# Performance work log

Measured on AMD Instinct MI355X. Metric: run time of the kernel, lower is better.

Reference implementation:

```python
import jax, jax.numpy as jnp
import numpy as np

SR = 8                      # search_range
MO = 2 * SR + 1             # max_offset = 17
NC = MO * MO                # 289 cost-volume channels


def _l2_normalize(x, eps=1e-12):
    # torch F.normalize(p=2, dim=1): x / max(||x||_2, eps)
    n = jnp.sqrt(jnp.sum(x * x, axis=1, keepdims=True))
    return x / jnp.maximum(n, eps)


def _conv2d(x, w, b, pad, groups=1):
    out = jax.lax.conv_general_dilated(
        x, w, window_strides=(1, 1), padding=[(pad, pad), (pad, pad)],
        feature_group_count=groups,
        dimension_numbers=('NCHW', 'OIHW', 'NCHW'))
    return out + b[None, :, None, None]


def _cost_volume(x1, x2, sr, norm_both=False):
    x1 = _l2_normalize(x1)
    if norm_both:
        x2 = _l2_normalize(x2)
    bs, c, h, w = x1.shape
    padded = jnp.pad(x2, ((0, 0), (0, 0), (sr, sr), (sr, sr)))
    mo = 2 * sr + 1
    # offsets in (j outer, i inner) order, matching the original double loop
    jj, ii = jnp.meshgrid(jnp.arange(mo), jnp.arange(mo), indexing='ij')
    offs = jnp.stack([jj.reshape(-1), ii.reshape(-1)], axis=-1)  # [mo^2, 2]

    def step(carry, off):
        sl = jax.lax.dynamic_slice(padded, (0, 0, off[0], off[1]), (bs, c, h, w))
        return carry, jnp.mean(x1 * sl, axis=1)  # [bs, h, w]

    _, cv = jax.lax.scan(step, None, offs)       # [mo^2, bs, h, w]
    cv = jnp.transpose(cv, (1, 0, 2, 3))          # [bs, mo^2, h, w]
    return jax.nn.leaky_relu(cv, 0.1)


def setup_inputs() -> dict:
    key = jax.random.key(0)
    ks = jax.random.split(key, 8)
    bs, c, h, w = 4, 256, 64, 64
    scale = 0.05
    return {
        'f1': jax.random.normal(ks[0], (bs, c, h, w), jnp.float32),
        'f2': jax.random.normal(ks[1], (bs, c, h, w), jnp.float32),
        'att_w': jax.random.normal(ks[2], (NC, 1, 7, 7), jnp.float32) * scale,
        'att_b': jax.random.normal(ks[3], (NC,), jnp.float32) * scale,
        'agg1_w': jax.random.normal(ks[4], (NC // 2, NC, 3, 3), jnp.float32) * scale,
        'agg1_b': jax.random.normal(ks[5], (NC // 2,), jnp.float32) * scale,
        'agg2_w': jax.random.normal(ks[6], (49, NC // 2, 3, 3), jnp.float32) * scale,
        'agg2_b': jax.random.normal(ks[7], (49,), jnp.float32) * scale,
    }


def reference(f1, f2, att_w, att_b, agg1_w, agg1_b, agg2_w, agg2_b):
    match_vol = _cost_volume(f1, f2, SR, norm_both=False)          # [bs,289,h,w]
    att = _conv2d(match_vol, att_w, att_b, pad=3, groups=NC)       # depthwise 7x7
    att_vol = match_vol * att
    h1 = jax.nn.relu(_conv2d(att_vol, agg1_w, agg1_b, pad=1))      # Conv(289->144,3)
    out = jax.nn.relu(_conv2d(h1, agg2_w, agg2_b, pad=1))          # Conv(144->49,3)
    return out
```

## Files before the change

### kernel.cpp

```cpp
#include <hip/hip_runtime.h>
#include <hip/hip_bf16.h>

#define BS   4
#define C    256
#define HW   4096
#define NPIX 16384
#define NCH  289
#define MO   17
#define PH   80
#define PW   80
#define C1   144
#define C2   49
#define ASTR 264
#define ICP  320
#define IC2  160
#define A2STR 168
#define CVP  70
#define CVC  320
#define CH64 72

typedef __bf16  bf16x8 __attribute__((ext_vector_type(8)));
typedef float   f32x4  __attribute__((ext_vector_type(4)));
typedef unsigned short us8 __attribute__((ext_vector_type(8)));

__global__ void fused_norm_transpose(const float* __restrict__ f1,
                                     unsigned short* __restrict__ dst) {
    __shared__ float tileT[32 * 257];
    __shared__ float invS[32];
    int blk = blockIdx.x;
    int pblk = blk & 127, b = blk >> 7;
    int p0 = pblk * 32;
    int t = threadIdx.x;
    int tx = t & 31, ty = t >> 5;
    const float* s = f1 + (size_t)b * C * HW;
#pragma unroll
    for (int i = 0; i < 32; ++i) {
        int c = ty + 8 * i;
        tileT[tx * 257 + c] = s[(size_t)c * HW + p0 + tx];
    }
    __syncthreads();
    int lane = t & 63, wave = t >> 6;
    int px = wave * 8 + (lane >> 3);
    int l = lane & 7;
    float ssum = 0.f;
#pragma unroll
    for (int j = 0; j < 32; ++j) {
        float v = tileT[px * 257 + l + 8 * j];
        ssum += v * v;
    }
    ssum += __shfl_xor(ssum, 1);
    ssum += __shfl_xor(ssum, 2);
    ssum += __shfl_xor(ssum, 4);
    if (l == 0) invS[px] = 1.0f / fmaxf(sqrtf(ssum), 1e-12f);
    __syncthreads();
#pragma unroll 4
    for (int p = 0; p < 32; ++p) {
        float v = tileT[p * 257 + t] * invS[p];
        __hip_bfloat16 hb = __float2bfloat16(v);
        dst[((size_t)b * HW + p0 + p) * C + t] = *(unsigned short*)&hb;
    }
}

__global__ void transpose_pad_kernel(const float* __restrict__ src,
                                     unsigned short* __restrict__ dst) {
    __shared__ float tile[32][33];
    int blk = blockIdx.x;
    int pblk = blk & 127;
    int cblk = (blk >> 7) & 7;
    int b    = blk >> 10;
    int tx = threadIdx.x & 31, ty = threadIdx.x >> 5;
    int c0 = cblk * 32, p0 = pblk * 32;
    const float* s = src + (size_t)b * C * HW;
#pragma unroll
    for (int i = 0; i < 4; ++i) {
        int c = c0 + ty + 8 * i;
        tile[ty + 8 * i][tx] = s[(size_t)c * HW + p0 + tx];
    }
    __syncthreads();
#pragma unroll
    for (int i = 0; i < 4; ++i) {
        int p = p0 + ty + 8 * i;
        float v = tile[tx][ty + 8 * i];
        int c = c0 + tx;
        int h = p >> 6, w = p & 63;
        __hip_bfloat16 hb = __float2bfloat16(v);
        dst[(((size_t)b * PH + h + 8) * PW + (w + 8)) * C + c] = *(unsigned short*)&hb;
    }
}

__global__ void halo_zero(unsigned short* __restrict__ p, int H, int halo, int Cc) {
    int W = H;
    int inter = H - 2 * halo;
    int total_pos = H * W - inter * inter;
    int chunks = Cc >> 3;
    size_t tot = (size_t)total_pos * chunks * BS;
    size_t idx = (size_t)blockIdx.x * 256 + threadIdx.x;
    if (idx >= tot) return;
    int c8 = (int)(idx % chunks);
    size_t r = idx / chunks;
    int pos = (int)(r % total_pos);
    int b = (int)(r / total_pos);
    int h, w;
    int topbot = 2 * halo * W;
    if (pos < halo * W) { h = pos / W; w = pos % W; }
    else if (pos < topbot) { int q = pos - halo * W; h = H - halo + q / W; w = q % W; }
    else {
        int q = pos - topbot;
        int row = q / (2 * halo), off = q % (2 * halo);
        h = halo + row;
        w = (off < halo) ? off : (W - 2 * halo + off);
    }
    us8 z = {0, 0, 0, 0, 0, 0, 0, 0};
    *(us8*)&p[(((size_t)b * H + h) * W + w) * Cc + c8 * 8] = z;
}

__global__ void rearrange_w1_bf(const float* __restrict__ w, unsigned short* __restrict__ wb) {
    int idx = blockIdx.x * 256 + threadIdx.x;
    if (idx >= 9 * C1 * ICP) return;
    int tap = idx / (C1 * ICP);
    int r = idx - tap * (C1 * ICP);
    int oc = r / ICP;
    int ic = r - oc * ICP;
    float v = (ic < NCH) ? w[((size_t)(oc * NCH + ic)) * 9 + tap] : 0.f;
    __hip_bfloat16 hb = __float2bfloat16(v);
    wb[idx] = *(unsigned short*)&hb;
}
__global__ void rearrange_w2_bf(const float* __restrict__ w, unsigned short* __restrict__ wb) {
    int idx = blockIdx.x * 256 + threadIdx.x;
    if (idx >= 9 * 64 * IC2) return;
    int tap = idx / (64 * IC2);
    int r = idx - tap * (64 * IC2);
    int oc = r / IC2;
    int ic = r - oc * IC2;
    float v = (oc < C2 && ic < C1) ? w[((size_t)(oc * C1 + ic)) * 9 + tap] : 0.f;
    __hip_bfloat16 hb = __float2bfloat16(v);
    wb[idx] = *(unsigned short*)&hb;
}
__global__ void rearrange_dw_pad(const float* __restrict__ w, float* __restrict__ wr) {
    int idx = blockIdx.x * 256 + threadIdx.x;
    if (idx >= 49 * CVC) return;
    int tap = idx / CVC;
    int ch = idx - tap * CVC;
    wr[idx] = (ch < NCH) ? w[ch * 49 + tap] : 0.f;
}

__global__ void cv_mfma_kernel(const unsigned short* __restrict__ x1b,
                               const unsigned short* __restrict__ x2b,
                               unsigned short* __restrict__ cvp) {
    __shared__ __align__(16) unsigned short x2s[2][32 * ASTR];
    int i = blockIdx.x;
    int xcd = i & 7;
    int j = i >> 3;
    int hq = xcd * 2 + (j & 1);
    int jj = j >> 1;
    int wseg = jj & 3;
    int b = jj >> 2;
    int h0 = hq * 4;
    int w0 = wseg * 16;
    int t = threadIdx.x;
    int wave = t >> 6, lane = t & 63;
    int lrow = lane & 15, quad = lane >> 4;
    int h = h0 + wave;

    const unsigned short* x1p = x1b + ((size_t)b * HW + h * 64 + w0) * C;
    bf16x8 a[8];
#pragma unroll
    for (int kk = 0; kk < 8; ++kk)
        a[kk] = *(const bf16x8*)&x1p[(size_t)lrow * C + kk * 32 + quad * 8];

    const unsigned short* x2base = x2b + (size_t)b * PH * PW * C;

    {
        const unsigned short* rowp = x2base + ((size_t)h0 * PW + w0) * C;
#pragma unroll
        for (int s = 0; s < 4; ++s) {
            int v = t + s * 256;
            int col = v >> 5, ch8 = v & 31;
            *(us8*)&x2s[0][col * ASTR + ch8 * 8] = *(const us8*)&rowp[(size_t)col * C + ch8 * 8];
        }
    }
    __syncthreads();

    for (int rr = 0; rr < 20; ++rr) {
        us8 pr[4];
        bool dop = (rr + 1 < 20);
        if (dop) {
            const unsigned short* rowp = x2base + ((size_t)(h0 + rr + 1) * PW + w0) * C;
#pragma unroll
            for (int s = 0; s < 4; ++s) {
                int v = t + s * 256;
                int col = v >> 5, ch8 = v & 31;
                pr[s] = *(const us8*)&rowp[(size_t)col * C + ch8 * 8];
            }
        }

        int dj = rr - wave;
        if ((unsigned)dj <= 16u) {
            const unsigned short* xs = x2s[rr & 1];
#pragma unroll
            for (int c = 0; c < 2; ++c) {
                f32x4 acc = {0.f, 0.f, 0.f, 0.f};
#pragma unroll
                for (int kk = 0; kk < 8; ++kk) {
                    bf16x8 bb = *(const bf16x8*)&xs[(c * 16 + lrow) * ASTR + kk * 32 + quad * 8];
                    acc = __builtin_amdgcn_mfma_f32_16x16x32_bf16(a[kk], bb, acc, 0, 0, 0);
                }
#pragma unroll
                for (int r = 0; r < 4; ++r) {
                    int px_l = quad * 4 + r;
                    int di = c * 16 + lrow - px_l;
                    if ((unsigned)di <= 16u) {
                        float v = acc[r] * (1.0f / 256.0f);
                        v = (v > 0.f) ? v : 0.1f * v;
                        __hip_bfloat16 hb = __float2bfloat16(v);
                        cvp[(((size_t)b * CVP + h + 3) * CVP + (w0 + px_l + 3)) * CVC + dj * MO + di] =
                            *(unsigned short*)&hb;
                    }
                }
            }
        }

        if (dop) {
            unsigned short* dst = x2s[(rr + 1) & 1];
#pragma unroll
            for (int s = 0; s < 4; ++s) {
                int v = t + s * 256;
                int col = v >> 5, ch8 = v & 31;
                *(us8*)&dst[col * ASTR + ch8 * 8] = pr[s];
            }
            __syncthreads();
        }
    }
}

__global__ void dw_att_tiled(const unsigned short* __restrict__ cvp,
                             const float* __restrict__ wdwp,
                             const float* __restrict__ att_b, unsigned short* __restrict__ av_pad) {
    __shared__ float actS[14 * 14 * 64];
    __shared__ float wdwS[49 * 64];
    int i = blockIdx.x;
    int ty = i & 7;
    int j = i >> 3;
    int cc = j % 5;
    int rest = j / 5;
    int tx = rest & 7, b = rest >> 3;
    int x0 = tx * 8, y0 = ty * 8;
    int c0 = cc * 64;
    int t = threadIdx.x;

    const unsigned short* cvb = cvp + (((size_t)b * CVP + y0) * CVP + x0) * CVC + c0;
    for (int v = t; v < 14 * 14 * 8; v += 256) {
        int rc = v >> 3, c8v = v & 7;
        int yy = rc / 14, xx = rc - yy * 14;
        bf16x8 raw = *(const bf16x8*)&cvb[((size_t)yy * CVP + xx) * CVC + c8v * 8];
        f32x4 lo, hi;
#pragma unroll
        for (int e = 0; e < 4; ++e) { lo[e] = (float)raw[e]; hi[e] = (float)raw[e + 4]; }
        *(f32x4*)&actS[rc * 64 + c8v * 8] = lo;
        *(f32x4*)&actS[rc * 64 + c8v * 8 + 4] = hi;
    }
    for (int v = t; v < 49 * 64; v += 256) {
        int tap = v >> 6, ch = v & 63;
        wdwS[v] = wdwp[tap * CVC + c0 + ch];
    }
    __syncthreads();

    int ch_l = t & 63, pgrp = t >> 6;
    int ch = c0 + ch_l;
    float bv = (ch < NCH) ? att_b[ch] : 0.f;
    float acc[16];
#pragma unroll
    for (int ii = 0; ii < 16; ++ii) acc[ii] = bv;

    for (int dy = 0; dy < 7; ++dy) {
#pragma unroll
        for (int dx = 0; dx < 7; ++dx) {
            float wv = wdwS[(dy * 7 + dx) * 64 + ch_l];
#pragma unroll
            for (int ii = 0; ii < 16; ++ii) {
                int py = pgrp * 2 + (ii >> 3), px = ii & 7;
                float a = actS[((py + dy) * 14 + (px + dx)) * 64 + ch_l];
                acc[ii] += a * wv;
            }
        }
    }

    if (ch < NCH) {
#pragma unroll
        for (int ii = 0; ii < 16; ++ii) {
            int py = pgrp * 2 + (ii >> 3), px = ii & 7;
            float c0v = actS[((py + 3) * 14 + (px + 3)) * 64 + ch_l];
            __hip_bfloat16 hb = __float2bfloat16(c0v * acc[ii]);
            av_pad[(((size_t)b * 66 + y0 + py + 1) * 66 + (x0 + px + 1)) * ICP + ch] =
                *(unsigned short*)&hb;
        }
    }
}

__global__ void agg1_mfma_kernel(const unsigned short* __restrict__ av_pad,
                                 const unsigned short* __restrict__ wb1,
                                 const float* __restrict__ bias,
                                 unsigned short* __restrict__ h1p) {
    __shared__ __align__(16) unsigned short aS2[2][66 * CH64];
    __shared__ __align__(16) unsigned short bS[2][C1 * CH64];
    int i = blockIdx.x;
    int xcd = i & 7;
    int j = i >> 3;
    int h = xcd * 8 + (j & 7);
    int b = j >> 3;
    int t = threadIdx.x;
    int wave = t >> 6, lane = t & 63;
    int lrow = lane & 15, quad = lane >> 4;
    int ot0 = (wave == 0) ? 0 : (wave * 2 + 1);
    int nt  = (wave == 0) ? 3 : 2;

    f32x4 acc[4][3];
#pragma unroll
    for (int m = 0; m < 4; ++m)
#pragma unroll
        for (int ii = 0; ii < 3; ++ii) acc[m][ii] = (f32x4){0.f, 0.f, 0.f, 0.f};

    const unsigned short* avb = av_pad + (((size_t)b * 66 + h) * 66) * ICP;

    {
        const unsigned short* arow = avb;
#pragma unroll
        for (int s = 0; s < 2; ++s) {
            int v = t + s * 256;
            *(us8*)&aS2[0][(v >> 3) * CH64 + (v & 7) * 8] =
                *(const us8*)&arow[(size_t)(v >> 3) * ICP + (v & 7) * 8];
        }
        if (t < 16) {
            int v = t + 512;
            *(us8*)&aS2[0][(v >> 3) * CH64 + (v & 7) * 8] =
                *(const us8*)&arow[(size_t)(v >> 3) * ICP + (v & 7) * 8];
        }
#pragma unroll
        for (int s = 0; s < 4; ++s) {
            int v = t + s * 256;
            *(us8*)&bS[0][(v >> 3) * CH64 + (v & 7) * 8] =
                *(const us8*)&wb1[(size_t)(v >> 3) * ICP + (v & 7) * 8];
        }
        if (t < 128) {
            int v = t + 1024;
            *(us8*)&bS[0][(v >> 3) * CH64 + (v & 7) * 8] =
                *(const us8*)&wb1[(size_t)(v >> 3) * ICP + (v & 7) * 8];
        }
    }
    __syncthreads();

    for (int k = 0; k < 45; ++k) {
        int rr = k % 15;
        int dx = rr % 3;
        int abuf = (k / 3) & 1, bbuf = k & 1;

        us8 br[5], ar[3];
        int kn = k + 1;
        bool do_b = (kn < 45);
        bool do_a = do_b && (kn % 3 == 0);
        int dyn = kn / 15, rn = kn % 15;
        int ccin = rn / 3, dxn = rn % 3;
        if (do_b) {
            const unsigned short* wt = wb1 + ((size_t)(dyn * 3 + dxn) * C1) * ICP + ccin * 64;
#pragma unroll
            for (int s = 0; s < 4; ++s) {
                int v = t + s * 256;
                br[s] = *(const us8*)&wt[(size_t)(v >> 3) * ICP + (v & 7) * 8];
            }
            if (t < 128) {
                int v = t + 1024;
                br[4] = *(const us8*)&wt[(size_t)(v >> 3) * ICP + (v & 7) * 8];
            }
        }
        if (do_a) {
            const unsigned short* arow = avb + (size_t)dyn * 66 * ICP + ccin * 64;
#pragma unroll
            for (int s = 0; s < 2; ++s) {
                int v = t + s * 256;
                ar[s] = *(const us8*)&arow[(size_t)(v >> 3) * ICP + (v & 7) * 8];
            }
            if (t < 16) {
                int v = t + 512;
                ar[2] = *(const us8*)&arow[(size_t)(v >> 3) * ICP + (v & 7) * 8];
            }
        }

        const unsigned short* aP = aS2[abuf];
        const unsigned short* bP = bS[bbuf];
#pragma unroll
        for (int cc2 = 0; cc2 < 2; ++cc2) {
            bf16x8 bfr[3];
#pragma unroll
            for (int ii = 0; ii < 3; ++ii)
                if (ii < nt)
                    bfr[ii] = *(const bf16x8*)&bP[((ot0 + ii) * 16 + lrow) * CH64 + cc2 * 32 + quad * 8];
#pragma unroll
            for (int m = 0; m < 4; ++m) {
                bf16x8 af = *(const bf16x8*)&aP[(m * 16 + lrow + dx) * CH64 + cc2 * 32 + quad * 8];
#pragma unroll
                for (int ii = 0; ii < 3; ++ii)
                    if (ii < nt)
                        acc[m][ii] = __builtin_amdgcn_mfma_f32_16x16x32_bf16(af, bfr[ii], acc[m][ii], 0, 0, 0);
            }
        }

        if (do_b) {
            unsigned short* dst = bS[bbuf ^ 1];
#pragma unroll
            for (int s = 0; s < 4; ++s) {
                int v = t + s * 256;
                *(us8*)&dst[(v >> 3) * CH64 + (v & 7) * 8] = br[s];
            }
            if (t < 128) {
                int v = t + 1024;
                *(us8*)&dst[(v >> 3) * CH64 + (v & 7) * 8] = br[4];
            }
        }
        if (do_a) {
            unsigned short* dst = aS2[abuf ^ 1];
#pragma unroll
            for (int s = 0; s < 2; ++s) {
                int v = t + s * 256;
                *(us8*)&dst[(v >> 3) * CH64 + (v & 7) * 8] = ar[s];
            }
            if (t < 16) {
                int v = t + 512;
                *(us8*)&dst[(v >> 3) * CH64 + (v & 7) * 8] = ar[2];
            }
        }
        if (do_b) __syncthreads();
    }

    size_t rowbase = ((size_t)b * 66 + h + 1) * 66;
#pragma unroll
    for (int m = 0; m < 4; ++m)
#pragma unroll
        for (int ii = 0; ii < 3; ++ii)
            if (ii < nt) {
                int oc = (ot0 + ii) * 16 + lrow;
                float bv = bias[oc];
#pragma unroll
                for (int r = 0; r < 4; ++r) {
                    int w = m * 16 + quad * 4 + r;
                    float val = fmaxf(acc[m][ii][r] + bv, 0.f);
                    __hip_bfloat16 hb = __float2bfloat16(val);
                    h1p[(rowbase + (w + 1)) * IC2 + oc] = *(unsigned short*)&hb;
                }
            }
}

__global__ void agg2_mfma_kernel(const unsigned short* __restrict__ h1p,
                                 const unsigned short* __restrict__ wb2,
                                 const float* __restrict__ bias, float* __restrict__ out) {
    __shared__ __align__(16) unsigned short aS[66 * A2STR];
    __shared__ __align__(16) unsigned short bS[64 * A2STR];
    int i = blockIdx.x;
    int xcd = i & 7;
    int j = i >> 3;
    int h = xcd * 8 + (j & 7);
    int b = j >> 3;
    int t = threadIdx.x;
    int wave = t >> 6, lane = t & 63;
    int lrow = lane & 15, quad = lane >> 4;
    int pt = wave;

    f32x4 acc[4];
#pragma unroll
    for (int ot = 0; ot < 4; ++ot) acc[ot] = (f32x4){0.f, 0.f, 0.f, 0.f};

    const unsigned short* h1b = h1p + (((size_t)b * 66 + h) * 66) * IC2;

    for (int dy = 0; dy < 3; ++dy) {
        __syncthreads();
        const unsigned short* arow = h1b + (size_t)dy * 66 * IC2;
        for (int v = t; v < 66 * (IC2 / 8); v += 256) {
            int col = v / (IC2 / 8);
            int c8 = v - col * (IC2 / 8);
            *(us8*)&aS[col * A2STR + c8 * 8] = *(const us8*)&arow[col * IC2 + c8 * 8];
        }
        for (int dx = 0; dx < 3; ++dx) {
            int tap = dy * 3 + dx;
            if (dx != 0) __syncthreads();
            const unsigned short* wtap = wb2 + (size_t)tap * 64 * IC2;
            for (int v = t; v < 64 * (IC2 / 8); v += 256) {
                int oc = v / (IC2 / 8);
                int c8 = v - oc * (IC2 / 8);
                *(us8*)&bS[oc * A2STR + c8 * 8] = *(const us8*)&wtap[(size_t)oc * IC2 + c8 * 8];
            }
            __syncthreads();
#pragma unroll
            for (int cc = 0; cc < 5; ++cc) {
                bf16x8 af = *(const bf16x8*)&aS[(pt * 16 + lrow + dx) * A2STR + cc * 32 + quad * 8];
#pragma unroll
                for (int ot = 0; ot < 4; ++ot) {
                    bf16x8 bfr = *(const bf16x8*)&bS[(ot * 16 + lrow) * A2STR + cc * 32 + quad * 8];
                    acc[ot] = __builtin_amdgcn_mfma_f32_16x16x32_bf16(af, bfr, acc[ot], 0, 0, 0);
                }
            }
        }
    }

#pragma unroll
    for (int ot = 0; ot < 4; ++ot) {
        int o = ot * 16 + lrow;
        if (o < C2) {
            float bv = bias[o];
#pragma unroll
            for (int r = 0; r < 4; ++r) {
                int w = pt * 16 + quad * 4 + r;
                out[((size_t)b * C2 + o) * HW + h * 64 + w] = fmaxf(acc[ot][r] + bv, 0.f);
            }
        }
    }
}

extern "C" void kernel_launch(void* const* d_in, const int* in_sizes, int n_in,
                              void* d_out, int out_size, void* d_ws, size_t ws_size,
                              hipStream_t stream) {
    const float* f1    = (const float*)d_in[0];
    const float* f2    = (const float*)d_in[1];
    const float* att_w = (const float*)d_in[2];
    const float* att_b = (const float*)d_in[3];
    const float* w1    = (const float*)d_in[4];
    const float* b1    = (const float*)d_in[5];
    const float* w2    = (const float*)d_in[6];
    const float* b2    = (const float*)d_in[7];
    float* out = (float*)d_out;

    char* wsb = (char*)d_ws;
    size_t off = 0;
    float* wdwp = (float*)(wsb + off); off += (size_t)49 * CVC * 4;
    off = (off + 15) & ~(size_t)15;
    unsigned short* x1bf = (unsigned short*)(wsb + off); off += (size_t)NPIX * C * 2;
    unsigned short* x2bf = (unsigned short*)(wsb + off); off += (size_t)BS * PH * PW * C * 2;
    unsigned short* cvp  = (unsigned short*)(wsb + off); off += (size_t)BS * CVP * CVP * CVC * 2;
    unsigned short* avp  = (unsigned short*)(wsb + off); off += (size_t)BS * 66 * 66 * ICP * 2;
    unsigned short* wb1  = (unsigned short*)(wsb + off); off += (size_t)9 * C1 * ICP * 2;
    unsigned short* h1p  = (unsigned short*)(wsb + off); off += (size_t)BS * 66 * 66 * IC2 * 2;
    unsigned short* wb2  = (unsigned short*)(wsb + off); off += (size_t)9 * 64 * IC2 * 2;
    if (ws_size < off) return;

    halo_zero<<<1152, 256, 0, stream>>>(x2bf, PH, 8, C);
    halo_zero<<<503, 256, 0, stream>>>(cvp, CVP, 3, CVC);
    halo_zero<<<163, 256, 0, stream>>>(avp, 66, 1, ICP);
    halo_zero<<<82, 256, 0, stream>>>(h1p, 66, 1, IC2);

    fused_norm_transpose<<<512, 256, 0, stream>>>(f1, x1bf);
    transpose_pad_kernel<<<4096, 256, 0, stream>>>(f2, x2bf);

    rearrange_w1_bf<<<(9 * C1 * ICP + 255) / 256, 256, 0, stream>>>(w1, wb1);
    rearrange_w2_bf<<<(9 * 64 * IC2 + 255) / 256, 256, 0, stream>>>(w2, wb2);
    rearrange_dw_pad<<<(49 * CVC + 255) / 256, 256, 0, stream>>>(att_w, wdwp);

    cv_mfma_kernel<<<256, 256, 0, stream>>>(x1bf, x2bf, cvp);
    dw_att_tiled<<<1280, 256, 0, stream>>>(cvp, wdwp, att_b, avp);
    agg1_mfma_kernel<<<256, 256, 0, stream>>>(avp, wb1, b1, h1p);
    agg2_mfma_kernel<<<256, 256, 0, stream>>>(h1p, wb2, b2, out);
}
```

Before: 213.3 us.

## Merge prep kernels into one launch and double-buffer agg2 loads

Seven small setup launches (halo zeroing and weight rearrangement) become one block-indexed prep kernel, which removes launch overhead. The agg2 conv now walks 27 steps of 64-channel chunks with double-buffered LDS. The next step's activation and weight chunks are prefetched into registers during the current MFMA work, and there is one barrier per step. The h1 channel stride is padded to 192 so the chunks divide evenly, which adds a few zero-channel MFMAs and raises register pressure.

New measurement: 195.5 us. 8.4% less time.

```diff
diff --git a/kernel.cpp b/kernel.cpp
--- a/kernel.cpp
+++ b/kernel.cpp
@@ -13,8 +13,7 @@
 #define C2   49
 #define ASTR 264
 #define ICP  320
-#define IC2  160
-#define A2STR 168
+#define IC3  192
 #define CVP  70
 #define CVC  320
 #define CH64 72
@@ -88,13 +87,14 @@
     }
 }
 
-__global__ void halo_zero(unsigned short* __restrict__ p, int H, int halo, int Cc) {
+__device__ __forceinline__ void halo_zero_dev(unsigned short* p, int H, int halo,
+                                              int Cc, int blk, int t) {
     int W = H;
     int inter = H - 2 * halo;
     int total_pos = H * W - inter * inter;
     int chunks = Cc >> 3;
     size_t tot = (size_t)total_pos * chunks * BS;
-    size_t idx = (size_t)blockIdx.x * 256 + threadIdx.x;
+    size_t idx = (size_t)blk * 256 + t;
     if (idx >= tot) return;
     int c8 = (int)(idx % chunks);
     size_t r = idx / chunks;
@@ -114,34 +114,46 @@
     *(us8*)&p[(((size_t)b * H + h) * W + w) * Cc + c8 * 8] = z;
 }
 
-__global__ void rearrange_w1_bf(const float* __restrict__ w, unsigned short* __restrict__ wb) {
-    int idx = blockIdx.x * 256 + threadIdx.x;
-    if (idx >= 9 * C1 * ICP) return;
-    int tap = idx / (C1 * ICP);
-    int r = idx - tap * (C1 * ICP);
-    int oc = r / ICP;
-    int ic = r - oc * ICP;
-    float v = (ic < NCH) ? w[((size_t)(oc * NCH + ic)) * 9 + tap] : 0.f;
-    __hip_bfloat16 hb = __float2bfloat16(v);
-    wb[idx] = *(unsigned short*)&hb;
-}
-__global__ void rearrange_w2_bf(const float* __restrict__ w, unsigned short* __restrict__ wb) {
-    int idx = blockIdx.x * 256 + threadIdx.x;
-    if (idx >= 9 * 64 * IC2) return;
-    int tap = idx / (64 * IC2);
-    int r = idx - tap * (64 * IC2);
-    int oc = r / IC2;
-    int ic = r - oc * IC2;
-    float v = (oc < C2 && ic < C1) ? w[((size_t)(oc * C1 + ic)) * 9 + tap] : 0.f;
-    __hip_bfloat16 hb = __float2bfloat16(v);
-    wb[idx] = *(unsigned short*)&hb;
-}
-__global__ void rearrange_dw_pad(const float* __restrict__ w, float* __restrict__ wr) {
-    int idx = blockIdx.x * 256 + threadIdx.x;
-    if (idx >= 49 * CVC) return;
-    int tap = idx / CVC;
-    int ch = idx - tap * CVC;
-    wr[idx] = (ch < NCH) ? w[ch * 49 + tap] : 0.f;
+__global__ void prep_kernel(unsigned short* __restrict__ x2bf, unsigned short* __restrict__ cvp,
+                            unsigned short* __restrict__ avp, unsigned short* __restrict__ h1p,
+                            const float* __restrict__ w1, unsigned short* __restrict__ wb1,
+                            const float* __restrict__ w2, unsigned short* __restrict__ wb2,
+                            const float* __restrict__ att_w, float* __restrict__ wdwp) {
+    int blk = blockIdx.x;
+    int t = threadIdx.x;
+    if (blk < 1152) { halo_zero_dev(x2bf, PH, 8, C, blk, t); return; }
+    if (blk < 1655) { halo_zero_dev(cvp, CVP, 3, CVC, blk - 1152, t); return; }
+    if (blk < 1818) { halo_zero_dev(avp, 66, 1, ICP, blk - 1655, t); return; }
+    if (blk < 1916) { halo_zero_dev(h1p, 66, 1, IC3, blk - 1818, t); return; }
+    if (blk < 3536) {
+        int idx = (blk - 1916) * 256 + t;
+        int tap = idx / (C1 * ICP);
+        int r = idx - tap * (C1 * ICP);
+        int oc = r / ICP;
+        int ic = r - oc * ICP;
+        float v = (ic < NCH) ? w1[((size_t)(oc * NCH + ic)) * 9 + tap] : 0.f;
+        __hip_bfloat16 hb = __float2bfloat16(v);
+        wb1[idx] = *(unsigned short*)&hb;
+        return;
+    }
+    if (blk < 3968) {
+        int idx = (blk - 3536) * 256 + t;
+        int tap = idx / (64 * IC3);
+        int r = idx - tap * (64 * IC3);
+        int oc = r / IC3;
+        int ic = r - oc * IC3;
+        float v = (oc < C2 && ic < C1) ? w2[((size_t)(oc * C1 + ic)) * 9 + tap] : 0.f;
+        __hip_bfloat16 hb = __float2bfloat16(v);
+        wb2[idx] = *(unsigned short*)&hb;
+        return;
+    }
+    {
+        int idx = (blk - 3968) * 256 + t;
+        if (idx >= 49 * CVC) return;
+        int tap = idx / CVC;
+        int ch = idx - tap * CVC;
+        wdwp[idx] = (ch < NCH) ? att_w[ch * 49 + tap] : 0.f;
+    }
 }
 
 __global__ void cv_mfma_kernel(const unsigned short* __restrict__ x1b,
@@ -444,7 +456,7 @@
                     int w = m * 16 + quad * 4 + r;
                     float val = fmaxf(acc[m][ii][r] + bv, 0.f);
                     __hip_bfloat16 hb = __float2bfloat16(val);
-                    h1p[(rowbase + (w + 1)) * IC2 + oc] = *(unsigned short*)&hb;
+                    h1p[(rowbase + (w + 1)) * IC3 + oc] = *(unsigned short*)&hb;
                 }
             }
 }
@@ -452,8 +464,8 @@
 __global__ void agg2_mfma_kernel(const unsigned short* __restrict__ h1p,
                                  const unsigned short* __restrict__ wb2,
                                  const float* __restrict__ bias, float* __restrict__ out) {
-    __shared__ __align__(16) unsigned short aS[66 * A2STR];
-    __shared__ __align__(16) unsigned short bS[64 * A2STR];
+    __shared__ __align__(16) unsigned short aS2[2][66 * CH64];
+    __shared__ __align__(16) unsigned short bS2[2][64 * CH64];
     int i = blockIdx.x;
     int xcd = i & 7;
     int j = i >> 3;
@@ -468,36 +480,94 @@
 #pragma unroll
     for (int ot = 0; ot < 4; ++ot) acc[ot] = (f32x4){0.f, 0.f, 0.f, 0.f};
 
-    const unsigned short* h1b = h1p + (((size_t)b * 66 + h) * 66) * IC2;
-
-    for (int dy = 0; dy < 3; ++dy) {
-        __syncthreads();
-        const unsigned short* arow = h1b + (size_t)dy * 66 * IC2;
-        for (int v = t; v < 66 * (IC2 / 8); v += 256) {
-            int col = v / (IC2 / 8);
-            int c8 = v - col * (IC2 / 8);
-            *(us8*)&aS[col * A2STR + c8 * 8] = *(const us8*)&arow[col * IC2 + c8 * 8];
-        }
-        for (int dx = 0; dx < 3; ++dx) {
-            int tap = dy * 3 + dx;
-            if (dx != 0) __syncthreads();
-            const unsigned short* wtap = wb2 + (size_t)tap * 64 * IC2;
-            for (int v = t; v < 64 * (IC2 / 8); v += 256) {
-                int oc = v / (IC2 / 8);
-                int c8 = v - oc * (IC2 / 8);
-                *(us8*)&bS[oc * A2STR + c8 * 8] = *(const us8*)&wtap[(size_t)oc * IC2 + c8 * 8];
-            }
-            __syncthreads();
-#pragma unroll
-            for (int cc = 0; cc < 5; ++cc) {
-                bf16x8 af = *(const bf16x8*)&aS[(pt * 16 + lrow + dx) * A2STR + cc * 32 + quad * 8];
-#pragma unroll
-                for (int ot = 0; ot < 4; ++ot) {
-                    bf16x8 bfr = *(const bf16x8*)&bS[(ot * 16 + lrow) * A2STR + cc * 32 + quad * 8];
-                    acc[ot] = __builtin_amdgcn_mfma_f32_16x16x32_bf16(af, bfr, acc[ot], 0, 0, 0);
-                }
-            }
-        }
+    const unsigned short* h1b = h1p + (((size_t)b * 66 + h) * 66) * IC3;
+
+    {
+#pragma unroll
+        for (int s = 0; s < 2; ++s) {
+            int v = t + s * 256;
+            *(us8*)&aS2[0][(v >> 3) * CH64 + (v & 7) * 8] =
+                *(const us8*)&h1b[(size_t)(v >> 3) * IC3 + (v & 7) * 8];
+        }
+        if (t < 16) {
+            int v = t + 512;
+            *(us8*)&aS2[0][(v >> 3) * CH64 + (v & 7) * 8] =
+                *(const us8*)&h1b[(size_t)(v >> 3) * IC3 + (v & 7) * 8];
+        }
+#pragma unroll
+        for (int s = 0; s < 2; ++s) {
+            int v = t + s * 256;
+            *(us8*)&bS2[0][(v >> 3) * CH64 + (v & 7) * 8] =
+                *(const us8*)&wb2[(size_t)(v >> 3) * IC3 + (v & 7) * 8];
+        }
+    }
+    __syncthreads();
+
+    for (int k = 0; k < 27; ++k) {
+        int rem = k % 9;
+        int dx = rem % 3;
+        int abuf = (k / 3) & 1, bbuf = k & 1;
+
+        us8 br[2], ar[3];
+        int kn = k + 1;
+        bool do_b = (kn < 27);
+        bool do_a = do_b && (kn % 3 == 0);
+        int dyn = kn / 9, rn = kn % 9;
+        int ccn = rn / 3, dxn = rn % 3;
+        if (do_b) {
+            const unsigned short* wt = wb2 + ((size_t)(dyn * 3 + dxn) * 64) * IC3 + ccn * 64;
+#pragma unroll
+            for (int s = 0; s < 2; ++s) {
+                int v = t + s * 256;
+                br[s] = *(const us8*)&wt[(size_t)(v >> 3) * IC3 + (v & 7) * 8];
+            }
+        }
+        if (do_a) {
+            const unsigned short* arow = h1b + (size_t)dyn * 66 * IC3 + ccn * 64;
+#pragma unroll
+            for (int s = 0; s < 2; ++s) {
+                int v = t + s * 256;
+                ar[s] = *(const us8*)&arow[(size_t)(v >> 3) * IC3 + (v & 7) * 8];
+            }
+            if (t < 16) {
+                int v = t + 512;
+                ar[2] = *(const us8*)&arow[(size_t)(v >> 3) * IC3 + (v & 7) * 8];
+            }
+        }
+
+        const unsigned short* aP = aS2[abuf];
+        const unsigned short* bP = bS2[bbuf];
+#pragma unroll
+        for (int cc2 = 0; cc2 < 2; ++cc2) {
+            bf16x8 af = *(const bf16x8*)&aP[(pt * 16 + lrow + dx) * CH64 + cc2 * 32 + quad * 8];
+#pragma unroll
+            for (int ot = 0; ot < 4; ++ot) {
+                bf16x8 bfr = *(const bf16x8*)&bP[(ot * 16 + lrow) * CH64 + cc2 * 32 + quad * 8];
+                acc[ot] = __builtin_amdgcn_mfma_f32_16x16x32_bf16(af, bfr, acc[ot], 0, 0, 0);
+            }
+        }
+
+        if (do_b) {
+            unsigned short* dst = bS2[bbuf ^ 1];
+#pragma unroll
+            for (int s = 0; s < 2; ++s) {
+                int v = t + s * 256;
+                *(us8*)&dst[(v >> 3) * CH64 + (v & 7) * 8] = br[s];
+            }
+        }
+        if (do_a) {
+            unsigned short* dst = aS2[abuf ^ 1];
+#pragma unroll
+            for (int s = 0; s < 2; ++s) {
+                int v = t + s * 256;
+                *(us8*)&dst[(v >> 3) * CH64 + (v & 7) * 8] = ar[s];
+            }
+            if (t < 16) {
+                int v = t + 512;
+                *(us8*)&dst[(v >> 3) * CH64 + (v & 7) * 8] = ar[2];
+            }
+        }
+        if (do_b) __syncthreads();
     }
 
 #pragma unroll
@@ -536,21 +606,13 @@
     unsigned short* cvp  = (unsigned short*)(wsb + off); off += (size_t)BS * CVP * CVP * CVC * 2;
     unsigned short* avp  = (unsigned short*)(wsb + off); off += (size_t)BS * 66 * 66 * ICP * 2;
     unsigned short* wb1  = (unsigned short*)(wsb + off); off += (size_t)9 * C1 * ICP * 2;
-    unsigned short* h1p  = (unsigned short*)(wsb + off); off += (size_t)BS * 66 * 66 * IC2 * 2;
-    unsigned short* wb2  = (unsigned short*)(wsb + off); off += (size_t)9 * 64 * IC2 * 2;
+    unsigned short* h1p  = (unsigned short*)(wsb + off); off += (size_t)BS * 66 * 66 * IC3 * 2;
+    unsigned short* wb2  = (unsigned short*)(wsb + off); off += (size_t)9 * 64 * IC3 * 2;
     if (ws_size < off) return;
 
-    halo_zero<<<1152, 256, 0, stream>>>(x2bf, PH, 8, C);
-    halo_zero<<<503, 256, 0, stream>>>(cvp, CVP, 3, CVC);
-    halo_zero<<<163, 256, 0, stream>>>(avp, 66, 1, ICP);
-    halo_zero<<<82, 256, 0, stream>>>(h1p, 66, 1, IC2);
-
+    prep_kernel<<<4030, 256, 0, stream>>>(x2bf, cvp, avp, h1p, w1, wb1, w2, wb2, att_w, wdwp);
     fused_norm_transpose<<<512, 256, 0, stream>>>(f1, x1bf);
     transpose_pad_kernel<<<4096, 256, 0, stream>>>(f2, x2bf);
-
-    rearrange_w1_bf<<<(9 * C1 * ICP + 255) / 256, 256, 0, stream>>>(w1, wb1);
-    rearrange_w2_bf<<<(9 * 64 * IC2 + 255) / 256, 256, 0, stream>>>(w2, wb2);
-    rearrange_dw_pad<<<(49 * CVC + 255) / 256, 256, 0, stream>>>(att_w, wdwp);
 
     cv_mfma_kernel<<<256, 256, 0, stream>>>(x1bf, x2bf, cvp);
     dw_att_tiled<<<1280, 256, 0, stream>>>(cvp, wdwp, att_b, avp);
```
